# Kernel optimization log

Hardware: AMD Instinct MI355X
Metric: run time of the kernel (lower is better)

The kernel has to match this reference:

```python
import jax, jax.numpy as jnp
import numpy as np


def setup_inputs() -> dict:
    key = jax.random.key(0)
    k1, k2 = jax.random.split(key)
    B, N, M, D = 8, 2048, 2048, 1024
    x = jax.random.normal(k1, (B, N, D), dtype=jnp.float32)
    y = jax.random.normal(k2, (B, M, D), dtype=jnp.float32)
    return {"x": x, "y": y}


def reference(x, y):
    # scores: [B, N, M] = x @ y^T
    scores = jnp.einsum("bnd,bmd->bnm", x, y)
    # row-normalized attention over M (axis=2 of scores)
    attn_row = jax.nn.softmax(scores, axis=2)
    # column-normalized attention: softmax over N of scores^T, i.e. axis=1 then transpose
    attn_col = jax.nn.softmax(scores, axis=1)  # [B, N, M], normalized over N
    A = jnp.einsum("bnm,bmd->bnd", attn_row, y)          # attended summary of y per x-token
    Bout = jnp.einsum("bnm,bnd->bmd", attn_col, x)       # attended summary of x per y-token
    return (A, Bout)
```

## Files before the change

kernel.cpp:

```cpp
#include <hip/hip_runtime.h>
#include <cstdint>
#include <cstddef>

namespace {

constexpr int Bb = 8;
constexpr int Nn = 2048;
constexpr int Dd = 1024;
constexpr int NT = 64;

typedef _Float16 half8 __attribute__((ext_vector_type(8)));
typedef float f32x2v __attribute__((ext_vector_type(2)));
typedef float f32x4v __attribute__((ext_vector_type(4)));
typedef float f32x16v __attribute__((ext_vector_type(16)));
typedef unsigned int v2u __attribute__((ext_vector_type(2)));
typedef unsigned int v4u __attribute__((ext_vector_type(4)));

__device__ __forceinline__ float fast_exp2(float x) {
  float r;
  asm("v_exp_f32 %0, %1\n\ts_nop 1" : "=v"(r) : "v"(x));
  return r;
}

__device__ __forceinline__ unsigned cvt2(float a, float b) {
  return __builtin_bit_cast(unsigned, __builtin_amdgcn_cvt_pkrtz(a, b));
}

template <int CTRL>
__device__ __forceinline__ float dpp_f(float v) {
  return __builtin_bit_cast(
      float, __builtin_amdgcn_update_dpp(0, __builtin_bit_cast(int, v), CTRL,
                                         0xF, 0xF, true));
}
__device__ __forceinline__ float red16_max(float v) {
  v = fmaxf(v, dpp_f<0xB1>(v));
  v = fmaxf(v, dpp_f<0x4E>(v));
  v = fmaxf(v, dpp_f<0x124>(v));
  v = fmaxf(v, dpp_f<0x128>(v));
  return v;
}
__device__ __forceinline__ float red16_add(float v) {
  v = v + dpp_f<0xB1>(v);
  v = v + dpp_f<0x4E>(v);
  v = v + dpp_f<0x124>(v);
  v = v + dpp_f<0x128>(v);
  return v;
}

__device__ __forceinline__ void barrier_lgkm() {
  asm volatile("s_waitcnt lgkmcnt(0)" ::: "memory");
  __builtin_amdgcn_s_barrier();
  __builtin_amdgcn_sched_barrier(0);
}
__device__ __forceinline__ void barrier_plain() {
  __builtin_amdgcn_s_barrier();
  __builtin_amdgcn_sched_barrier(0);
}

__global__ void convf16(const float* __restrict__ in, v4u* __restrict__ out) {
  const int n8 = Bb * Nn * Dd / 8;
  int i = blockIdx.x * blockDim.x + threadIdx.x;
  const int stride = gridDim.x * blockDim.x;
  const f32x4v* in4 = (const f32x4v*)in;
  for (; i < n8; i += stride) {
    f32x4v a = in4[2 * i], b = in4[2 * i + 1];
    v4u p;
    p[0] = cvt2(a[0], a[1]);
    p[1] = cvt2(a[2], a[3]);
    p[2] = cvt2(b[0], b[1]);
    p[3] = cvt2(b[2], b[3]);
    out[i] = p;
  }
}

template <int WS>
__device__ __forceinline__ v4u ld8h(const float* f32p, const v4u* h16p) {
  if constexpr (WS) {
    return *h16p;
  } else {
    f32x4v a = *(const f32x4v*)f32p;
    f32x4v b = *(const f32x4v*)(f32p + 4);
    v4u p;
    p[0] = cvt2(a[0], a[1]);
    p[1] = cvt2(a[2], a[3]);
    p[2] = cvt2(b[0], b[1]);
    p[3] = cvt2(b[2], b[3]);
    return p;
  }
}

template <int WS>
__global__ __launch_bounds__(512, 2) void flash_fwd(
    const float* __restrict__ Qf, const float* __restrict__ Yf,
    const v4u* __restrict__ Qw, const v4u* __restrict__ Yw,
    float* __restrict__ Om) {
  __shared__ __attribute__((aligned(128))) char ybuf[65536];
  __shared__ __attribute__((aligned(16))) float pscr2[4][32][36];
  __shared__ __attribute__((aligned(16))) char Pb[2048];
  __shared__ float sscale[32];
  __shared__ float sinvl[32];
  __shared__ __attribute__((aligned(16))) int sflag8[8];

  const int tid = (int)threadIdx.x;
  const int w = tid >> 6, l = tid & 63;
  const int lm = l & 15, g = (l >> 4) & 3, g2 = (l >> 5) & 1, l31 = l & 31;
  const int kvf = w >> 2, ds = w & 3;
  const int bid = (int)blockIdx.x, batch = bid & 7, row0 = (bid >> 3) * 32;
  const size_t bY = (size_t)batch * Nn;

  v4u qreg[2][8];
#pragma unroll
  for (int qh = 0; qh < 2; ++qh)
#pragma unroll
    for (int ks = 0; ks < 8; ++ks) {
      const int rr = row0 + qh * 16 + lm;
      const int dd_ = ds * 256 + ks * 32 + g * 8;
      qreg[qh][ks] = ld8h<WS>(Qf + (size_t)(bY + rr) * Dd + dd_,
                              Qw + (size_t)(bY + rr) * 128 + (dd_ >> 3));
    }

#define LOADY(dst, t_)                                                        \
  do {                                                                        \
    const int rr_ = (t_)*32 + kvf * 16 + lm;                                  \
    _Pragma("unroll") for (int ks = 0; ks < 8; ++ks) {                        \
      const int dd_ = ds * 256 + ks * 32 + g * 8;                             \
      dst[ks] = ld8h<WS>(Yf + (size_t)(bY + rr_) * Dd + dd_,                  \
                         Yw + (size_t)(bY + rr_) * 128 + (dd_ >> 3));         \
    }                                                                         \
  } while (0)

  const unsigned sbase =
      (unsigned)((kvf * 4 + (lm >> 2)) * 8192 + (ds * 16 + (g >> 1)) * 128 +
                 (lm & 3) * 32 + (g & 1) * 16);
#define STAGE_WR(SRC)                                                         \
  do {                                                                        \
    _Pragma("unroll") for (int ks = 0; ks < 8; ++ks)                          \
        *(v4u*)(ybuf + sbase + ks * 256) = SRC[ks];                           \
  } while (0)

  v4u s[8];
  LOADY(s, 0);
  STAGE_WR(s);

  f32x16v Oacc[4];
#pragma unroll
  for (int i = 0; i < 4; ++i)
#pragma unroll
    for (int j = 0; j < 16; ++j) Oacc[i][j] = 0.0f;

  float m_run = -__builtin_inff();
  float l_run = 0.0f;
  const unsigned ylds = (unsigned)(uintptr_t)&ybuf[0];
  constexpr float L2E = 1.44269504088896f;

  v2u trr[16];

#define ISSUE_TR()                                                            \
  do {                                                                        \
    _Pragma("unroll") for (int kb = 0; kb < 2; ++kb)                          \
        _Pragma("unroll") for (int df = 0; df < 4; ++df) {                    \
      const unsigned wb =                                                     \
          ylds + (unsigned)((kb * 4 + g2 * 2) * 8192 +                        \
                            ((w * 4 + df) * 2 + (l31 >> 4)) * 128 +           \
                            (l31 & 15) * 8);                                  \
      asm volatile("ds_read_b64_tr_b16 %0, %1"                                \
                   : "=v"(trr[kb * 8 + df * 2])                               \
                   : "v"(wb));                                                \
      asm volatile("ds_read_b64_tr_b16 %0, %1"                                \
                   : "=v"(trr[kb * 8 + df * 2 + 1])                           \
                   : "v"(wb + 8192u));                                        \
    }                                                                         \
  } while (0)

  __syncthreads();

#define TILE_BODY(t_)                                                         \
  do {                                                                        \
    f32x4v acc0 = {0.f, 0.f, 0.f, 0.f}, acc1 = {0.f, 0.f, 0.f, 0.f};          \
    _Pragma("unroll") for (int ks = 0; ks < 8; ++ks) {                        \
      half8 av = __builtin_bit_cast(half8, s[ks]);                            \
      acc0 = __builtin_amdgcn_mfma_f32_16x16x32_f16(                          \
          av, __builtin_bit_cast(half8, qreg[0][ks]), acc0, 0, 0, 0);         \
      acc1 = __builtin_amdgcn_mfma_f32_16x16x32_f16(                          \
          av, __builtin_bit_cast(half8, qreg[1][ks]), acc1, 0, 0, 0);         \
    }                                                                         \
    LOADY(s, ((t_) + 1) & 63);                                                \
    *(f32x4v*)&pscr2[ds][lm][kvf * 16 + g * 4] = acc0;                        \
    *(f32x4v*)&pscr2[ds][16 + lm][kvf * 16 + g * 4] = acc1;                   \
    barrier_lgkm();                       \
    {                   \
      const int rq = 4 * w + (l >> 4);                             \
      const int c = l & 15;                      \
      float s0 = 0.f, s1 = 0.f;                                               \
      _Pragma("unroll") for (int sl = 0; sl < 4; ++sl) {                      \
        f32x2v p_ = *(const f32x2v*)&pscr2[sl][rq][2 * c];                    \
        s0 += p_[0];                                                          \
        s1 += p_[1];                                                          \
      }                                                                       \
      float pm = red16_max(fmaxf(s0, s1));                                    \
      bool defer = (pm <= m_run + 8.0f);                                      \
      bool allw = (bool)__all((int)defer);                                    \
      float scale = 1.0f;                                                     \
      if (!allw) {                                                            \
        float mn = fmaxf(m_run, pm);                                          \
        scale = fast_exp2((m_run - mn) * L2E);                                \
        m_run = mn;                                                           \
      }                                                                       \
      float e0 = fast_exp2((s0 - m_run) * L2E);                               \
      float e1 = fast_exp2((s1 - m_run) * L2E);                               \
      float ps = red16_add(e0 + e1);                                          \
      l_run = l_run * scale + ps;                                             \
      *(unsigned*)(Pb + (c >> 2) * 512 + rq * 16 + (c & 3) * 4) =             \
          cvt2(e0, e1);                                                       \
      if (c == 0) sscale[rq] = scale;                                         \
      if (l == 0) sflag8[w] = allw ? 0 : 1;                                   \
    }                                                                         \
    ISSUE_TR();                                                               \
    barrier_lgkm();               \
    half8 pa0 = *(const half8*)(Pb + g2 * 512 + l31 * 16);                    \
    half8 pa1 = *(const half8*)(Pb + (2 + g2) * 512 + l31 * 16);              \
    v4u f0 = *(const v4u*)&sflag8[0];                                         \
    v4u f1 = *(const v4u*)&sflag8[4];                                         \
    if (f0[0] | f0[1] | f0[2] | f0[3] | f1[0] | f1[1] | f1[2] | f1[3]) {      \
      _Pragma("unroll") for (int df = 0; df < 4; ++df)                        \
          _Pragma("unroll") for (int r = 0; r < 16; ++r) {                    \
        const int q_ = (r & 3) + 8 * (r >> 2) + 4 * g2;                       \
        Oacc[df][r] *= sscale[q_];                                            \
      }                                                                       \
    }                                                                         \
    asm volatile("s_waitcnt lgkmcnt(0)" ::: "memory");                        \
    __builtin_amdgcn_sched_barrier(0);                                        \
    _Pragma("unroll") for (int kb = 0; kb < 2; ++kb)                          \
        _Pragma("unroll") for (int df = 0; df < 4; ++df) {                    \
      v4u bu;                                                                 \
      bu[0] = trr[kb * 8 + df * 2][0];                                        \
      bu[1] = trr[kb * 8 + df * 2][1];                                        \
      bu[2] = trr[kb * 8 + df * 2 + 1][0];                                    \
      bu[3] = trr[kb * 8 + df * 2 + 1][1];                                    \
      Oacc[df] = __builtin_amdgcn_mfma_f32_32x32x16_f16(                      \
          kb ? pa1 : pa0, __builtin_bit_cast(half8, bu), Oacc[df], 0, 0, 0);  \
    }                                                                         \
    barrier_plain();                \
    STAGE_WR(s);                                                              \
  } while (0)

  for (int t = 0; t < NT; ++t) {
    TILE_BODY(t);
  }

  if ((l & 15) == 0) sinvl[4 * w + (l >> 4)] = 1.0f / l_run;
  __syncthreads();
#pragma unroll
  for (int df = 0; df < 4; ++df)
#pragma unroll
    for (int r = 0; r < 16; ++r) {
      const int q_ = (r & 3) + 8 * (r >> 2) + 4 * g2;
      const float inv = sinvl[q_];
      Om[(size_t)(bY + row0 + q_) * Dd + (w * 4 + df) * 32 + l31] =
          Oacc[df][r] * inv;
    }
#undef TILE_BODY
#undef ISSUE_TR
#undef STAGE_WR
#undef LOADY
}

}

extern "C" void kernel_launch(void* const* d_in, const int* in_sizes, int n_in,
                              void* d_out, int out_size, void* d_ws,
                              size_t ws_size, hipStream_t stream) {
  (void)in_sizes; (void)n_in; (void)out_size;
  const float* x = (const float*)d_in[0];
  const float* y = (const float*)d_in[1];
  float* A = (float*)d_out;
  float* Bo = A + (size_t)Bb * Nn * Dd;
  const size_t halfws = (size_t)Bb * Nn * Dd * 2;
  dim3 fg(512), fb(512);
  if (d_ws != nullptr && ws_size >= 2 * halfws) {
    v4u* Xw = (v4u*)d_ws;
    v4u* Yw = (v4u*)((char*)d_ws + halfws);
    hipLaunchKernelGGL(convf16, dim3(2048), dim3(256), 0, stream, x, Xw);
    hipLaunchKernelGGL(convf16, dim3(2048), dim3(256), 0, stream, y, Yw);
    hipLaunchKernelGGL(flash_fwd<1>, fg, fb, 0, stream, x, y, Xw, Yw, A);
    hipLaunchKernelGGL(flash_fwd<1>, fg, fb, 0, stream, y, x, Yw, Xw, Bo);
  } else {
    hipLaunchKernelGGL(flash_fwd<0>, fg, fb, 0, stream, x, y, (const v4u*)x,
                       (const v4u*)y, A);
    hipLaunchKernelGGL(flash_fwd<0>, fg, fb, 0, stream, y, x, (const v4u*)y,
                       (const v4u*)x, Bo);
  }
}
```

Baseline: 547.6 us.

## Software-pipeline flash loop with double-buffered Y tile and P buffers

Splits the tile loop so the PV MFMA for tile t-1 runs alongside the QK^T MFMAs for tile t. The Y staging buffer and the P buffer become double-buffered to carry this, and one barrier per iteration is removed. The aim is to hide LDS transpose-read latency and the softmax-to-PV dependency behind independent MFMA work. The cost is that LDS use roughly doubles to about 150KB per block, which likely drops occupancy from two blocks per CU to one.

```diff
diff --git a/kernel.cpp b/kernel.cpp
--- a/kernel.cpp
+++ b/kernel.cpp
@@ -94,9 +94,9 @@
     const float* __restrict__ Qf, const float* __restrict__ Yf,
     const v4u* __restrict__ Qw, const v4u* __restrict__ Yw,
     float* __restrict__ Om) {
-  __shared__ __attribute__((aligned(128))) char ybuf[65536];
+  __shared__ __attribute__((aligned(128))) char ybuf[2][65536];
   __shared__ __attribute__((aligned(16))) float pscr2[4][32][36];
-  __shared__ __attribute__((aligned(16))) char Pb[2048];
+  __shared__ __attribute__((aligned(16))) char Pb[2][2048];
   __shared__ float sscale[32];
   __shared__ float sinvl[32];
   __shared__ __attribute__((aligned(16))) int sflag8[8];
@@ -132,51 +132,31 @@
   const unsigned sbase =
       (unsigned)((kvf * 4 + (lm >> 2)) * 8192 + (ds * 16 + (g >> 1)) * 128 +
                  (lm & 3) * 32 + (g & 1) * 16);
-#define STAGE_WR(SRC)                                                         \
+#define STAGE_WR(SRC, BASE)                                                   \
   do {                                                                        \
     _Pragma("unroll") for (int ks = 0; ks < 8; ++ks)                          \
-        *(v4u*)(ybuf + sbase + ks * 256) = SRC[ks];                           \
-  } while (0)
-
-  v4u s[8];
-  LOADY(s, 0);
-  STAGE_WR(s);
-
-  f32x16v Oacc[4];
-#pragma unroll
-  for (int i = 0; i < 4; ++i)
-#pragma unroll
-    for (int j = 0; j < 16; ++j) Oacc[i][j] = 0.0f;
-
-  float m_run = -__builtin_inff();
-  float l_run = 0.0f;
-  const unsigned ylds = (unsigned)(uintptr_t)&ybuf[0];
-  constexpr float L2E = 1.44269504088896f;
-
-  v2u trr[16];
-
-#define ISSUE_TR()                                                            \
+        *(v4u*)((BASE) + sbase + ks * 256) = SRC[ks];                         \
+  } while (0)
+
+#define ISSUE_TR(DST, TRBASE)                                                 \
   do {                                                                        \
     _Pragma("unroll") for (int kb = 0; kb < 2; ++kb)                          \
         _Pragma("unroll") for (int df = 0; df < 4; ++df) {                    \
       const unsigned wb =                                                     \
-          ylds + (unsigned)((kb * 4 + g2 * 2) * 8192 +                        \
-                            ((w * 4 + df) * 2 + (l31 >> 4)) * 128 +           \
-                            (l31 & 15) * 8);                                  \
+          (TRBASE) + (unsigned)((kb * 4 + g2 * 2) * 8192 +                    \
+                                ((w * 4 + df) * 2 + (l31 >> 4)) * 128 +       \
+                                (l31 & 15) * 8);                              \
       asm volatile("ds_read_b64_tr_b16 %0, %1"                                \
-                   : "=v"(trr[kb * 8 + df * 2])                               \
+                   : "=v"(DST[kb * 8 + df * 2])                               \
                    : "v"(wb));                                                \
       asm volatile("ds_read_b64_tr_b16 %0, %1"                                \
-                   : "=v"(trr[kb * 8 + df * 2 + 1])                           \
+                   : "=v"(DST[kb * 8 + df * 2 + 1])                           \
                    : "v"(wb + 8192u));                                        \
     }                                                                         \
   } while (0)
 
-  __syncthreads();
-
-#define TILE_BODY(t_)                                                         \
-  do {                                                                        \
-    f32x4v acc0 = {0.f, 0.f, 0.f, 0.f}, acc1 = {0.f, 0.f, 0.f, 0.f};          \
+#define S_BLOCK()                                                             \
+  do {                                                                        \
     _Pragma("unroll") for (int ks = 0; ks < 8; ++ks) {                        \
       half8 av = __builtin_bit_cast(half8, s[ks]);                            \
       acc0 = __builtin_amdgcn_mfma_f32_16x16x32_f16(                          \
@@ -184,43 +164,39 @@
       acc1 = __builtin_amdgcn_mfma_f32_16x16x32_f16(                          \
           av, __builtin_bit_cast(half8, qreg[1][ks]), acc1, 0, 0, 0);         \
     }                                                                         \
-    LOADY(s, ((t_) + 1) & 63);                                                \
-    *(f32x4v*)&pscr2[ds][lm][kvf * 16 + g * 4] = acc0;                        \
-    *(f32x4v*)&pscr2[ds][16 + lm][kvf * 16 + g * 4] = acc1;                   \
-    barrier_lgkm();                       \
-    {                   \
-      const int rq = 4 * w + (l >> 4);                             \
-      const int c = l & 15;                      \
-      float s0 = 0.f, s1 = 0.f;                                               \
-      _Pragma("unroll") for (int sl = 0; sl < 4; ++sl) {                      \
-        f32x2v p_ = *(const f32x2v*)&pscr2[sl][rq][2 * c];                    \
-        s0 += p_[0];                                                          \
-        s1 += p_[1];                                                          \
-      }                                                                       \
-      float pm = red16_max(fmaxf(s0, s1));                                    \
-      bool defer = (pm <= m_run + 8.0f);                                      \
-      bool allw = (bool)__all((int)defer);                                    \
-      float scale = 1.0f;                                                     \
-      if (!allw) {                                                            \
-        float mn = fmaxf(m_run, pm);                                          \
-        scale = fast_exp2((m_run - mn) * L2E);                                \
-        m_run = mn;                                                           \
-      }                                                                       \
-      float e0 = fast_exp2((s0 - m_run) * L2E);                               \
-      float e1 = fast_exp2((s1 - m_run) * L2E);                               \
-      float ps = red16_add(e0 + e1);                                          \
-      l_run = l_run * scale + ps;                                             \
-      *(unsigned*)(Pb + (c >> 2) * 512 + rq * 16 + (c & 3) * 4) =             \
-          cvt2(e0, e1);                                                       \
-      if (c == 0) sscale[rq] = scale;                                         \
-      if (l == 0) sflag8[w] = allw ? 0 : 1;                                   \
-    }                                                                         \
-    ISSUE_TR();                                                               \
-    barrier_lgkm();               \
-    half8 pa0 = *(const half8*)(Pb + g2 * 512 + l31 * 16);                    \
-    half8 pa1 = *(const half8*)(Pb + (2 + g2) * 512 + l31 * 16);              \
-    v4u f0 = *(const v4u*)&sflag8[0];                                         \
-    v4u f1 = *(const v4u*)&sflag8[4];                                         \
+  } while (0)
+
+#define SOFTMAX(PBW)                                                          \
+  do {                                                                        \
+    const int rq = 4 * w + (l >> 4);                               \
+    const int c = l & 15;                        \
+    float s0 = 0.f, s1 = 0.f;                                                 \
+    _Pragma("unroll") for (int sl = 0; sl < 4; ++sl) {                        \
+      f32x2v p_ = *(const f32x2v*)&pscr2[sl][rq][2 * c];                      \
+      s0 += p_[0];                                                            \
+      s1 += p_[1];                                                            \
+    }                                                                         \
+    float pm = red16_max(fmaxf(s0, s1));                                      \
+    bool defer = (pm <= m_run + 8.0f);                                        \
+    bool allw = (bool)__all((int)defer);                                      \
+    float scale = 1.0f;                                                       \
+    if (!allw) {                                                              \
+      float mn = fmaxf(m_run, pm);                                            \
+      scale = fast_exp2((m_run - mn) * L2E);                                  \
+      m_run = mn;                                                             \
+    }                                                                         \
+    float e0 = fast_exp2((s0 - m_run) * L2E);                                 \
+    float e1 = fast_exp2((s1 - m_run) * L2E);                                 \
+    float ps = red16_add(e0 + e1);                                            \
+    l_run = l_run * scale + ps;                                               \
+    *(unsigned*)((PBW) + (c >> 2) * 512 + rq * 16 + (c & 3) * 4) =            \
+        cvt2(e0, e1);                                                         \
+    if (c == 0) sscale[rq] = scale;                                           \
+    if (l == 0) sflag8[w] = allw ? 0 : 1;                                     \
+  } while (0)
+
+#define PV_MFMA()                                                             \
+  do {                                                                        \
     if (f0[0] | f0[1] | f0[2] | f0[3] | f1[0] | f1[1] | f1[2] | f1[3]) {      \
       _Pragma("unroll") for (int df = 0; df < 4; ++df)                        \
           _Pragma("unroll") for (int r = 0; r < 16; ++r) {                    \
@@ -228,8 +204,6 @@
         Oacc[df][r] *= sscale[q_];                                            \
       }                                                                       \
     }                                                                         \
-    asm volatile("s_waitcnt lgkmcnt(0)" ::: "memory");                        \
-    __builtin_amdgcn_sched_barrier(0);                                        \
     _Pragma("unroll") for (int kb = 0; kb < 2; ++kb)                          \
         _Pragma("unroll") for (int df = 0; df < 4; ++df) {                    \
       v4u bu;                                                                 \
@@ -240,12 +214,78 @@
       Oacc[df] = __builtin_amdgcn_mfma_f32_32x32x16_f16(                      \
           kb ? pa1 : pa0, __builtin_bit_cast(half8, bu), Oacc[df], 0, 0, 0);  \
     }                                                                         \
-    barrier_plain();                \
-    STAGE_WR(s);                                                              \
-  } while (0)
-
-  for (int t = 0; t < NT; ++t) {
-    TILE_BODY(t);
+  } while (0)
+
+  char* const yb0 = &ybuf[0][0];
+  const unsigned ylds = (unsigned)(uintptr_t)yb0;
+  constexpr float L2E = 1.44269504088896f;
+
+  v4u s[8];
+  LOADY(s, 0);
+  STAGE_WR(s, yb0);
+
+  f32x16v Oacc[4];
+#pragma unroll
+  for (int i = 0; i < 4; ++i)
+#pragma unroll
+    for (int j = 0; j < 16; ++j) Oacc[i][j] = 0.0f;
+
+  float m_run = -__builtin_inff();
+  float l_run = 0.0f;
+
+  __syncthreads();
+
+  {
+    f32x4v acc0 = {0.f, 0.f, 0.f, 0.f}, acc1 = {0.f, 0.f, 0.f, 0.f};
+    S_BLOCK();
+    LOADY(s, 1);
+    *(f32x4v*)&pscr2[ds][lm][kvf * 16 + g * 4] = acc0;
+    *(f32x4v*)&pscr2[ds][16 + lm][kvf * 16 + g * 4] = acc1;
+    barrier_lgkm();
+    SOFTMAX(&Pb[0][0]);
+    STAGE_WR(s, yb0 + 65536);
+    barrier_lgkm();
+  }
+
+  for (int t = 1; t < NT; ++t) {
+    const unsigned trbase = ylds + (unsigned)(((t - 1) & 1) * 65536);
+    char* const ybn = yb0 + (((t + 1) & 1) * 65536);
+    const char* pbp = &Pb[(t - 1) & 1][0];
+    char* const pbw = &Pb[t & 1][0];
+
+    half8 pa0 = *(const half8*)(pbp + g2 * 512 + l31 * 16);
+    half8 pa1 = *(const half8*)(pbp + (2 + g2) * 512 + l31 * 16);
+    v4u f0 = *(const v4u*)&sflag8[0];
+    v4u f1 = *(const v4u*)&sflag8[4];
+    v2u trr[16];
+    ISSUE_TR(trr, trbase);
+    f32x4v acc0 = {0.f, 0.f, 0.f, 0.f}, acc1 = {0.f, 0.f, 0.f, 0.f};
+    S_BLOCK();
+    LOADY(s, (t + 1) & 63);
+    *(f32x4v*)&pscr2[ds][lm][kvf * 16 + g * 4] = acc0;
+    *(f32x4v*)&pscr2[ds][16 + lm][kvf * 16 + g * 4] = acc1;
+    asm volatile("s_waitcnt lgkmcnt(0)" ::: "memory");
+    __builtin_amdgcn_sched_barrier(0);
+    PV_MFMA();
+    barrier_plain();
+
+    SOFTMAX(pbw);
+    STAGE_WR(s, ybn);
+    barrier_lgkm();
+  }
+
+  {
+    const unsigned trbase = ylds + 65536u;
+    const char* pbp = &Pb[1][0];
+    half8 pa0 = *(const half8*)(pbp + g2 * 512 + l31 * 16);
+    half8 pa1 = *(const half8*)(pbp + (2 + g2) * 512 + l31 * 16);
+    v4u f0 = *(const v4u*)&sflag8[0];
+    v4u f1 = *(const v4u*)&sflag8[4];
+    v2u trr[16];
+    ISSUE_TR(trr, trbase);
+    asm volatile("s_waitcnt lgkmcnt(0)" ::: "memory");
+    __builtin_amdgcn_sched_barrier(0);
+    PV_MFMA();
   }
 
   if ((l & 15) == 0) sinvl[4 * w + (l >> 4)] = 1.0f / l_run;
@@ -259,7 +299,9 @@
       Om[(size_t)(bY + row0 + q_) * Dd + (w * 4 + df) * 32 + l31] =
           Oacc[df][r] * inv;
     }
-#undef TILE_BODY
+#undef PV_MFMA
+#undef SOFTMAX
+#undef S_BLOCK
 #undef ISSUE_TR
 #undef STAGE_WR
 #undef LOADY
```

Measured after the change: 675.6 us. 1.23x slower.
